# Kernel tuning notes

Hardware: AMD Instinct MI355X
Metric: run time of the kernel (lower is better)

## Reference

```python
import jax, jax.numpy as jnp
import numpy as np

RATES = (6, 12, 18, 24)  # dilation/padding per branch


def _offset_conv(x, w, b, rate):
    # mmcv ConvModule with norm_cfg=None: conv (bias=True) + ReLU
    y = jax.lax.conv_general_dilated(
        x, w, window_strides=(1, 1),
        padding=[(rate, rate), (rate, rate)],
        rhs_dilation=(rate, rate),
        dimension_numbers=('NCHW', 'OIHW', 'NCHW'))
    return jax.nn.relu(y + b[None, :, None, None])


def _deform_conv(x, offset, w, rate):
    # DCNv1: 3x3 deformable conv, stride 1, padding=dilation=rate,
    # deformable_groups=1, no bias. Zero padding outside image (bilinear).
    B, C, H, W = x.shape
    K = 9  # 3x3 kernel taps, row-major; offset channels [2k]=dy, [2k+1]=dx
    ky = (jnp.arange(K) // 3 - 1).astype(x.dtype)
    kx = (jnp.arange(K) % 3 - 1).astype(x.dtype)
    off = offset.reshape(B, K, 2, H, W)
    gy = jnp.arange(H, dtype=x.dtype)
    gx = jnp.arange(W, dtype=x.dtype)
    # sampling coords [B,K,H,W]: p0 + dilated kernel offset + learned offset
    py = gy[None, None, :, None] + ky[None, :, None, None] * rate + off[:, :, 0]
    px = gx[None, None, None, :] + kx[None, :, None, None] * rate + off[:, :, 1]
    y0 = jnp.floor(py)
    x0 = jnp.floor(px)
    wy = (py - y0)[:, None]  # [B,1,K,H,W]
    wx = (px - x0)[:, None]
    y0i = y0.astype(jnp.int32)
    x0i = x0.astype(jnp.int32)
    xf = x.reshape(B, C, H * W)

    def gather(yi, xi):
        valid = (yi >= 0) & (yi < H) & (xi >= 0) & (xi < W)
        idx = (jnp.clip(yi, 0, H - 1) * W + jnp.clip(xi, 0, W - 1)).reshape(B, K * H * W)
        v = jnp.take_along_axis(xf, idx[:, None, :], axis=2).reshape(B, C, K, H, W)
        return v * valid[:, None].astype(x.dtype)

    samp = (gather(y0i, x0i) * (1 - wy) * (1 - wx)
            + gather(y0i, x0i + 1) * (1 - wy) * wx
            + gather(y0i + 1, x0i) * wy * (1 - wx)
            + gather(y0i + 1, x0i + 1) * wy * wx)  # [B,C,K,H,W]
    return jnp.einsum('oik,bikhw->bohw', w.reshape(w.shape[0], C, K), samp)


def setup_inputs() -> dict:
    key = jax.random.key(0)
    k1, k2, k3 = jax.random.split(key, 3)
    B, C, H, W = 2, 256, 64, 64
    Cout, R = 256, len(RATES)
    x = jax.random.normal(k1, (B, C, H, W), dtype=jnp.float32)
    dweights = jax.random.normal(k2, (R, Cout, C, 3, 3), dtype=jnp.float32) * 0.02
    oweights = jax.random.normal(k3, (R, 18, C, 3, 3), dtype=jnp.float32) * 0.01
    obias = jnp.zeros((R, 18), dtype=jnp.float32)
    return {"x": x, "dweights": dweights, "oweights": oweights, "obias": obias}


def reference(x, dweights, oweights, obias):
    R = len(RATES)
    outs = []
    for i in range(R):
        j = (i - 1) % R  # source quirk: offsets[i-1] (wraps to last for i=0)
        off = _offset_conv(x, oweights[j], obias[j], RATES[j])
        outs.append(_deform_conv(x, off, dweights[i], RATES[i]))
    return jnp.concatenate(outs, axis=1)
```

## Files before the change

### kernel.cpp

```cpp
#include <hip/hip_runtime.h>
#include <hip/hip_bf16.h>

typedef __attribute__((ext_vector_type(4))) float f32x4;
typedef __attribute__((ext_vector_type(2))) _Float16 h2;
typedef __attribute__((ext_vector_type(8))) _Float16 f16x8;

__global__ __launch_bounds__(256) void transpose_x_hwc_f16(const float* __restrict__ x,
                                                           unsigned short* __restrict__ x16h) {
    __shared__ float s[64][65];
    int blk = blockIdx.x;
    int b = blk >> 8, ct = (blk >> 6) & 3, pt = blk & 63;
    int c0 = ct * 64, p0 = pt * 64;
    int tid = threadIdx.x;
    int tr = tid >> 6, tc = tid & 63;
#pragma unroll
    for (int i = 0; i < 16; ++i) {
        int c = i * 4 + tr;
        s[c][tc] = x[((size_t)b * 256 + c0 + c) * 4096 + p0 + tc];
    }
    __syncthreads();
#pragma unroll
    for (int i = 0; i < 16; ++i) {
        int pp = i * 4 + tr;
        _Float16 h = (_Float16)s[tc][pp];
        x16h[((size_t)b * 4096 + p0 + pp) * 256 + c0 + tc] = *(unsigned short*)&h;
    }
}

__global__ __launch_bounds__(256) void transpose_dw_f16(const float* __restrict__ dw,
                                                        unsigned short* __restrict__ wTh) {
    int idx = blockIdx.x * 256 + threadIdx.x;
    int c = idx & 255;
    int o = (idx >> 8) & 255;
    int rest = idx >> 16;
    int k = rest % 9, i = rest / 9;
    _Float16 h = (_Float16)dw[(((i << 8) + o) * 256 + c) * 9 + k];
    wTh[idx] = *(unsigned short*)&h;
}

__global__ __launch_bounds__(256) void transpose_ow_f16(const float* __restrict__ ow,
                                                        unsigned short* __restrict__ owTh) {
    int idx = blockIdx.x * 256 + threadIdx.x;
    int c = idx & 255;
    int m = (idx >> 8) & 31;
    int rk = idx >> 13;
    int k = rk % 9, r = rk / 9;
    float v = (m < 18) ? ow[((r * 18 + m) * 256 + c) * 9 + k] : 0.f;
    _Float16 h = (_Float16)v;
    owTh[idx] = *(unsigned short*)&h;
}

__global__ __launch_bounds__(512) void offset_mfma2f(const unsigned short* __restrict__ x16h,
                                                     const unsigned short* __restrict__ owTh,
                                                     const float* __restrict__ obias,
                                                     float* __restrict__ off) {
    __shared__ short    s_a[4][32][8];
    __shared__ short    s_b[4][128][8];
    __shared__ int      s_pix[9][128];
    __shared__ unsigned s_msk[9][128];

    const int blk = blockIdx.x;
    const int r = (blk & 7) >> 1, b = blk & 1;
    const int px0 = (blk >> 3) << 7;
    const int rate = 6 * (r + 1);

    const int tid = threadIdx.x;
    const int lane = tid & 63;
    const int w = tid >> 6;
    const int kg = lane >> 4, lm = lane & 15;
    const int sg = tid >> 7, spx = tid & 127;
    const int mA = (tid & 127) >> 2, kgA = tid & 3;

    const unsigned short* xbh = x16h + (size_t)b * 1048576;
    const unsigned short* wrb = owTh + (size_t)r * 9 * 32 * 256;

    for (int e = tid; e < 1152; e += 512) {
        int k = e >> 7, pl = e & 127;
        int pg = px0 + pl;
        int yy = (pg >> 6) + (k / 3 - 1) * rate;
        int xx = (pg & 63) + (k % 3 - 1) * rate;
        bool v = ((unsigned)yy < 64u) && ((unsigned)xx < 64u);
        int cy = min(max(yy, 0), 63), cx = min(max(xx, 0), 63);
        s_pix[k][pl] = cy * 64 + cx;
        s_msk[k][pl] = v ? 0xFFFFFFFFu : 0u;
    }
    __syncthreads();

    f32x4 acc0 = (f32x4)(0.f), acc1 = (f32x4)(0.f);

    uint4 a, v;
    if (tid < 128) a = *(const uint4*)(wrb + (size_t)mA * 256 + kgA * 8);
    {
        int pix = s_pix[0][spx];
        v = *(const uint4*)(xbh + (size_t)pix * 256 + sg * 8);
    }
    unsigned m = s_msk[0][spx];

    for (int t = 0; t < 72; ++t) {
        uint4 pk = make_uint4(v.x & m, v.y & m, v.z & m, v.w & m);

        __syncthreads();
        if (tid < 128) *(uint4*)&s_a[kgA][mA][0] = a;
        *(uint4*)&s_b[sg][spx][0] = pk;
        __syncthreads();

        if (t < 71) {
            int tn = t + 1, tapn = tn >> 3, c0n = (tn & 7) << 5;
            if (tid < 128)
                a = *(const uint4*)(wrb + ((size_t)tapn * 32 + mA) * 256 + c0n + kgA * 8);
            int pix = s_pix[tapn][spx];
            m = s_msk[tapn][spx];
            v = *(const uint4*)(xbh + (size_t)pix * 256 + c0n + sg * 8);
        }

        f16x8 bf  = *(const f16x8*)&s_b[kg][w * 16 + lm][0];
        f16x8 af0 = *(const f16x8*)&s_a[kg][lm][0];
        f16x8 af1 = *(const f16x8*)&s_a[kg][16 + lm][0];
        acc0 = __builtin_amdgcn_mfma_f32_16x16x32_f16(af0, bf, acc0, 0, 0, 0);
        acc1 = __builtin_amdgcn_mfma_f32_16x16x32_f16(af1, bf, acc1, 0, 0, 0);
    }

    const float* bias = obias + r * 18;
    float* ob = off + (size_t)(r * 2 + b) * 18 * 4096;
    int px = px0 + w * 16 + lm;
#pragma unroll
    for (int reg = 0; reg < 4; ++reg) {
        int mm = kg * 4 + reg;
        ob[(size_t)mm * 4096 + px] = fmaxf(acc0[reg] + bias[mm], 0.f);
        int m1 = 16 + mm;
        if (m1 < 18)
            ob[(size_t)m1 * 4096 + px] = fmaxf(acc1[reg] + bias[m1], 0.f);
    }
}

__global__ __launch_bounds__(512, 2) void deform_mfma7(const unsigned short* __restrict__ x16h,
                                                       const unsigned short* __restrict__ wTh,
                                                       const float* __restrict__ off,
                                                       float* __restrict__ out) {
    __shared__ short  s_a[256][64];
    __shared__ short  s_b[64][64];
    __shared__ int4   s_pix[9][64];
    __shared__ float4 s_wt[9][64];

    const int blk = blockIdx.x;
    const int i = (blk & 7) >> 1, b = blk & 1;
    const int px0 = (blk >> 3) << 6;
    const int r = (i + 3) & 3;
    const int rate = 6 * (i + 1);

    const int tid = threadIdx.x;
    const int lane = tid & 63;
    const int w = tid >> 6;
    const int wo = w >> 1, wp = w & 1;
    const int kg = lane >> 4, lm = lane & 15;
    const int pxS = tid >> 3, chgS = tid & 7;
    const int oA = tid >> 3, partA = tid & 7;
    const int colA = (partA * 8) ^ ((oA & 7) * 8);

    const unsigned short* xbh = x16h + (size_t)b * 1048576;
    const float* offb = off + (size_t)(r * 2 + b) * 18 * 4096;
    const unsigned short* wib = wTh + (size_t)i * 9 * 65536;

    for (int e = tid; e < 576; e += 512) {
        int k = e >> 6, pl = e & 63;
        int pg = px0 + pl;
        int yy = pg >> 6, xc = pg & 63;
        float dy = offb[(size_t)(2 * k) * 4096 + pg];
        float dx = offb[(size_t)(2 * k + 1) * 4096 + pg];
        float py = (float)(yy + (k / 3 - 1) * rate) + dy;
        float pxf = (float)(xc + (k % 3 - 1) * rate) + dx;
        float fy = floorf(py), fx = floorf(pxf);
        int y0 = (int)fy, x0 = (int)fx;
        float wy = py - fy, wx = pxf - fx;
        float vy0 = ((unsigned)y0 < 64u) ? 1.f : 0.f;
        float vy1 = ((unsigned)(y0 + 1) < 64u) ? 1.f : 0.f;
        float vx0 = ((unsigned)x0 < 64u) ? 1.f : 0.f;
        float vx1 = ((unsigned)(x0 + 1) < 64u) ? 1.f : 0.f;
        int cy0 = min(max(y0, 0), 63), cy1 = min(max(y0 + 1, 0), 63);
        int cx0 = min(max(x0, 0), 63), cx1 = min(max(x0 + 1, 0), 63);
        s_pix[k][pl] = make_int4(cy0 * 64 + cx0, cy0 * 64 + cx1,
                                 cy1 * 64 + cx0, cy1 * 64 + cx1);
        s_wt[k][pl] = make_float4(vy0 * vx0 * (1.f - wy) * (1.f - wx),
                                  vy0 * vx1 * (1.f - wy) * wx,
                                  vy1 * vx0 * wy * (1.f - wx),
                                  vy1 * vx1 * wy * wx);
    }
    __syncthreads();

    f32x4 acc[4][2];
#pragma unroll
    for (int mi = 0; mi < 4; ++mi) {
        acc[mi][0] = (f32x4)(0.f);
        acc[mi][1] = (f32x4)(0.f);
    }

    uint4 a0, a1, a2, a3, v0, v1, v2, v3;
    {
        const unsigned short* wrow = wib + partA * 8;
        a0 = *(const uint4*)(wrow + (size_t)(oA      ) * 256);
        a1 = *(const uint4*)(wrow + (size_t)(oA +  64) * 256);
        a2 = *(const uint4*)(wrow + (size_t)(oA + 128) * 256);
        a3 = *(const uint4*)(wrow + (size_t)(oA + 192) * 256);
        int4 p = s_pix[0][pxS];
        const unsigned short* xch = xbh + chgS * 8;
        v0 = *(const uint4*)(xch + ((size_t)p.x << 8));
        v1 = *(const uint4*)(xch + ((size_t)p.y << 8));
        v2 = *(const uint4*)(xch + ((size_t)p.z << 8));
        v3 = *(const uint4*)(xch + ((size_t)p.w << 8));
    }

    for (int t = 0; t < 36; ++t) {
        const int tap = t >> 2;

        uint4 pk;
        {
            float4 qwf = s_wt[tap][pxS];
            h2 qx = (h2)((_Float16)qwf.x), qy = (h2)((_Float16)qwf.y);
            h2 qz = (h2)((_Float16)qwf.z), qv = (h2)((_Float16)qwf.w);
            h2 r0 = (*(h2*)&v0.x) * qx + (*(h2*)&v1.x) * qy + (*(h2*)&v2.x) * qz + (*(h2*)&v3.x) * qv;
            h2 r1 = (*(h2*)&v0.y) * qx + (*(h2*)&v1.y) * qy + (*(h2*)&v2.y) * qz + (*(h2*)&v3.y) * qv;
            h2 r2 = (*(h2*)&v0.z) * qx + (*(h2*)&v1.z) * qy + (*(h2*)&v2.z) * qz + (*(h2*)&v3.z) * qv;
            h2 r3 = (*(h2*)&v0.w) * qx + (*(h2*)&v1.w) * qy + (*(h2*)&v2.w) * qz + (*(h2*)&v3.w) * qv;
            pk = make_uint4(*(unsigned*)&r0, *(unsigned*)&r1, *(unsigned*)&r2, *(unsigned*)&r3);
        }

        __syncthreads();
        *(uint4*)&s_a[oA      ][colA] = a0;
        *(uint4*)&s_a[oA +  64][colA] = a1;
        *(uint4*)&s_a[oA + 128][colA] = a2;
        *(uint4*)&s_a[oA + 192][colA] = a3;
        *(uint4*)&s_b[pxS][(chgS ^ (pxS & 7)) * 8] = pk;
        __syncthreads();

        if (t < 35) {
            int tn = t + 1, tapn = tn >> 2, c0n = (tn & 3) << 6;
            const unsigned short* wrow = wib + (size_t)tapn * 65536 + c0n + partA * 8;
            a0 = *(const uint4*)(wrow + (size_t)(oA      ) * 256);
            a1 = *(const uint4*)(wrow + (size_t)(oA +  64) * 256);
            a2 = *(const uint4*)(wrow + (size_t)(oA + 128) * 256);
            a3 = *(const uint4*)(wrow + (size_t)(oA + 192) * 256);
            int4 p = s_pix[tapn][pxS];
            const unsigned short* xch = xbh + c0n + chgS * 8;
            v0 = *(const uint4*)(xch + ((size_t)p.x << 8));
            v1 = *(const uint4*)(xch + ((size_t)p.y << 8));
            v2 = *(const uint4*)(xch + ((size_t)p.z << 8));
            v3 = *(const uint4*)(xch + ((size_t)p.w << 8));
        }

#pragma unroll
        for (int kf = 0; kf < 2; ++kf) {
            int oct = kf * 4 + kg;
            int bcol = (oct ^ (lm & 7)) * 8;
            f16x8 bf0 = *(const f16x8*)&s_b[wp * 32 + lm][bcol];
            f16x8 bf1 = *(const f16x8*)&s_b[wp * 32 + 16 + lm][bcol];
#pragma unroll
            for (int mi = 0; mi < 4; ++mi) {
                int o = wo * 64 + mi * 16 + lm;
                int col = (oct * 8) ^ ((o & 7) * 8);
                f16x8 af = *(const f16x8*)&s_a[o][col];
                acc[mi][0] = __builtin_amdgcn_mfma_f32_16x16x32_f16(af, bf0, acc[mi][0], 0, 0, 0);
                acc[mi][1] = __builtin_amdgcn_mfma_f32_16x16x32_f16(af, bf1, acc[mi][1], 0, 0, 0);
            }
        }
    }

    float* ob = out + ((size_t)b * 1024 + i * 256) * 4096;
#pragma unroll
    for (int mi = 0; mi < 4; ++mi) {
        int o = wo * 64 + mi * 16 + kg * 4;
#pragma unroll
        for (int ni = 0; ni < 2; ++ni) {
            int pg = px0 + wp * 32 + ni * 16 + lm;
#pragma unroll
            for (int reg = 0; reg < 4; ++reg)
                ob[(size_t)(o + reg) * 4096 + pg] = acc[mi][ni][reg];
        }
    }
}

extern "C" void kernel_launch(void* const* d_in, const int* in_sizes, int n_in,
                              void* d_out, int out_size, void* d_ws, size_t ws_size,
                              hipStream_t stream) {
    const float* x  = (const float*)d_in[0];
    const float* dw = (const float*)d_in[1];
    const float* ow = (const float*)d_in[2];
    const float* ob = (const float*)d_in[3];
    float* out = (float*)d_out;

    float* ws  = (float*)d_ws;
    float* off = ws;
    unsigned short* wTh  = (unsigned short*)(ws + 589824);
    unsigned short* owTh = wTh + 2359296;
    unsigned short* x16h = (unsigned short*)(ws + 1916928);

    transpose_x_hwc_f16<<<512, 256, 0, stream>>>(x, x16h);
    transpose_dw_f16<<<9216, 256, 0, stream>>>(dw, wTh);
    transpose_ow_f16<<<1152, 256, 0, stream>>>(ow, owTh);
    offset_mfma2f<<<256, 512, 0, stream>>>(x16h, owTh, ob, off);
    deform_mfma7<<<512, 512, 0, stream>>>(x16h, wTh, off, out);
}
```

Measured before the change: 113.9 us.

## Load deform-conv weight fragments directly to registers and double-buffer sampled tile

The deform kernel no longer stages the weight (A) tile through shared memory. Each lane loads its MFMA A-fragments straight from global memory into registers. The sampled-input (B) tile is now double-buffered in LDS, which lets the two block barriers per iteration become one raw s_barrier. The goal is less LDS traffic, fewer writes and fewer syncs. In exchange, global weight loads are less coalesced and there are more of them per block, since each wave fetches its own 64-row slice, and register pressure rises.

```diff
diff --git a/kernel.cpp b/kernel.cpp
--- a/kernel.cpp
+++ b/kernel.cpp
@@ -133,12 +133,15 @@
     }
 }
 
-__global__ __launch_bounds__(512, 2) void deform_mfma7(const unsigned short* __restrict__ x16h,
+#define MFMA2(AF, B0, B1, M)                                                            \
+    acc[M][0] = __builtin_amdgcn_mfma_f32_16x16x32_f16(*(const f16x8*)&AF, B0, acc[M][0], 0, 0, 0); \
+    acc[M][1] = __builtin_amdgcn_mfma_f32_16x16x32_f16(*(const f16x8*)&AF, B1, acc[M][1], 0, 0, 0);
+
+__global__ __launch_bounds__(512, 2) void deform_mfma8(const unsigned short* __restrict__ x16h,
                                                        const unsigned short* __restrict__ wTh,
                                                        const float* __restrict__ off,
                                                        float* __restrict__ out) {
-    __shared__ short  s_a[256][64];
-    __shared__ short  s_b[64][64];
+    __shared__ short  s_b[2][64][64];
     __shared__ int4   s_pix[9][64];
     __shared__ float4 s_wt[9][64];
 
@@ -154,12 +157,11 @@
     const int wo = w >> 1, wp = w & 1;
     const int kg = lane >> 4, lm = lane & 15;
     const int pxS = tid >> 3, chgS = tid & 7;
-    const int oA = tid >> 3, partA = tid & 7;
-    const int colA = (partA * 8) ^ ((oA & 7) * 8);
 
     const unsigned short* xbh = x16h + (size_t)b * 1048576;
     const float* offb = off + (size_t)(r * 2 + b) * 18 * 4096;
     const unsigned short* wib = wTh + (size_t)i * 9 * 65536;
+    const unsigned short* wlane = wib + (size_t)(wo * 64 + lm) * 256 + kg * 8;
 
     for (int e = tid; e < 576; e += 512) {
         int k = e >> 6, pl = e & 63;
@@ -194,13 +196,17 @@
         acc[mi][1] = (f32x4)(0.f);
     }
 
-    uint4 a0, a1, a2, a3, v0, v1, v2, v3;
+    uint4 a00, a01, a02, a03, a10, a11, a12, a13, v0, v1, v2, v3;
     {
-        const unsigned short* wrow = wib + partA * 8;
-        a0 = *(const uint4*)(wrow + (size_t)(oA      ) * 256);
-        a1 = *(const uint4*)(wrow + (size_t)(oA +  64) * 256);
-        a2 = *(const uint4*)(wrow + (size_t)(oA + 128) * 256);
-        a3 = *(const uint4*)(wrow + (size_t)(oA + 192) * 256);
+        const unsigned short* wb = wlane;
+        a00 = *(const uint4*)(wb);
+        a01 = *(const uint4*)(wb + 4096);
+        a02 = *(const uint4*)(wb + 8192);
+        a03 = *(const uint4*)(wb + 12288);
+        a10 = *(const uint4*)(wb + 32);
+        a11 = *(const uint4*)(wb + 4096 + 32);
+        a12 = *(const uint4*)(wb + 8192 + 32);
+        a13 = *(const uint4*)(wb + 12288 + 32);
         int4 p = s_pix[0][pxS];
         const unsigned short* xch = xbh + chgS * 8;
         v0 = *(const uint4*)(xch + ((size_t)p.x << 8));
@@ -209,6 +215,7 @@
         v3 = *(const uint4*)(xch + ((size_t)p.w << 8));
     }
 
+    int buf = 0;
     for (int t = 0; t < 36; ++t) {
         const int tap = t >> 2;
 
@@ -223,22 +230,12 @@
             h2 r3 = (*(h2*)&v0.w) * qx + (*(h2*)&v1.w) * qy + (*(h2*)&v2.w) * qz + (*(h2*)&v3.w) * qv;
             pk = make_uint4(*(unsigned*)&r0, *(unsigned*)&r1, *(unsigned*)&r2, *(unsigned*)&r3);
         }
-
-        __syncthreads();
-        *(uint4*)&s_a[oA      ][colA] = a0;
-        *(uint4*)&s_a[oA +  64][colA] = a1;
-        *(uint4*)&s_a[oA + 128][colA] = a2;
-        *(uint4*)&s_a[oA + 192][colA] = a3;
-        *(uint4*)&s_b[pxS][(chgS ^ (pxS & 7)) * 8] = pk;
-        __syncthreads();
+        *(uint4*)&s_b[buf][pxS][(chgS ^ (pxS & 7)) * 8] = pk;
+
+        asm volatile("s_waitcnt lgkmcnt(0)\n\ts_barrier" ::: "memory");
 
         if (t < 35) {
             int tn = t + 1, tapn = tn >> 2, c0n = (tn & 3) << 6;
-            const unsigned short* wrow = wib + (size_t)tapn * 65536 + c0n + partA * 8;
-            a0 = *(const uint4*)(wrow + (size_t)(oA      ) * 256);
-            a1 = *(const uint4*)(wrow + (size_t)(oA +  64) * 256);
-            a2 = *(const uint4*)(wrow + (size_t)(oA + 128) * 256);
-            a3 = *(const uint4*)(wrow + (size_t)(oA + 192) * 256);
             int4 p = s_pix[tapn][pxS];
             const unsigned short* xch = xbh + c0n + chgS * 8;
             v0 = *(const uint4*)(xch + ((size_t)p.x << 8));
@@ -247,21 +244,36 @@
             v3 = *(const uint4*)(xch + ((size_t)p.w << 8));
         }
 
-#pragma unroll
-        for (int kf = 0; kf < 2; ++kf) {
-            int oct = kf * 4 + kg;
-            int bcol = (oct ^ (lm & 7)) * 8;
-            f16x8 bf0 = *(const f16x8*)&s_b[wp * 32 + lm][bcol];
-            f16x8 bf1 = *(const f16x8*)&s_b[wp * 32 + 16 + lm][bcol];
-#pragma unroll
-            for (int mi = 0; mi < 4; ++mi) {
-                int o = wo * 64 + mi * 16 + lm;
-                int col = (oct * 8) ^ ((o & 7) * 8);
-                f16x8 af = *(const f16x8*)&s_a[o][col];
-                acc[mi][0] = __builtin_amdgcn_mfma_f32_16x16x32_f16(af, bf0, acc[mi][0], 0, 0, 0);
-                acc[mi][1] = __builtin_amdgcn_mfma_f32_16x16x32_f16(af, bf1, acc[mi][1], 0, 0, 0);
-            }
-        }
+        {
+            int bcol0 = (kg ^ (lm & 7)) * 8;
+            int bcol1 = ((kg + 4) ^ (lm & 7)) * 8;
+            f16x8 b00 = *(const f16x8*)&s_b[buf][wp * 32 + lm][bcol0];
+            f16x8 b01 = *(const f16x8*)&s_b[buf][wp * 32 + 16 + lm][bcol0];
+            MFMA2(a00, b00, b01, 0)
+            MFMA2(a01, b00, b01, 1)
+            MFMA2(a02, b00, b01, 2)
+            MFMA2(a03, b00, b01, 3)
+            f16x8 b10 = *(const f16x8*)&s_b[buf][wp * 32 + lm][bcol1];
+            f16x8 b11 = *(const f16x8*)&s_b[buf][wp * 32 + 16 + lm][bcol1];
+            MFMA2(a10, b10, b11, 0)
+            MFMA2(a11, b10, b11, 1)
+            MFMA2(a12, b10, b11, 2)
+            MFMA2(a13, b10, b11, 3)
+        }
+
+        if (t < 35) {
+            int tn = t + 1, tapn = tn >> 2, c0n = (tn & 3) << 6;
+            const unsigned short* wb = wlane + (size_t)tapn * 65536 + c0n;
+            a00 = *(const uint4*)(wb);
+            a01 = *(const uint4*)(wb + 4096);
+            a02 = *(const uint4*)(wb + 8192);
+            a03 = *(const uint4*)(wb + 12288);
+            a10 = *(const uint4*)(wb + 32);
+            a11 = *(const uint4*)(wb + 4096 + 32);
+            a12 = *(const uint4*)(wb + 8192 + 32);
+            a13 = *(const uint4*)(wb + 12288 + 32);
+        }
+        buf ^= 1;
     }
 
     float* ob = out + ((size_t)b * 1024 + i * 256) * 4096;
@@ -297,5 +309,5 @@
     transpose_dw_f16<<<9216, 256, 0, stream>>>(dw, wTh);
     transpose_ow_f16<<<1152, 256, 0, stream>>>(ow, owTh);
     offset_mfma2f<<<256, 512, 0, stream>>>(x16h, owTh, ob, off);
-    deform_mfma7<<<512, 512, 0, stream>>>(x16h, wTh, off, out);
-}
+    deform_mfma8<<<512, 512, 0, stream>>>(x16h, wTh, off, out);
+}
```

Measured after the change: 209.1 us. 1.84x slower.
